# Optimization experiments

Hardware: AMD Instinct MI355X
Metric: run time of the kernel (lower is better)

## Reference

```python
import jax, jax.numpy as jnp
import numpy as np
from jax import lax


def _conv(x, w, b, pad, dil):
    # standard dense conv, NCHW / OIHW
    out = lax.conv_general_dilated(
        x, w, window_strides=(1, 1), padding=[(pad, pad), (pad, pad)],
        rhs_dilation=(dil, dil), dimension_numbers=('NCHW', 'OIHW', 'NCHW'))
    return out + b[None, :, None, None]


def _bilinear_sample(x, py, px):
    # x: [B,C,H,W]; py,px: [B,H,W] float coords. Zero padding outside bounds
    # (matches torchvision deform_conv2d bilinear sampling).
    B, C, H, W = x.shape
    y0 = jnp.floor(py)
    x0 = jnp.floor(px)
    wy = (py - y0)[:, None]  # [B,1,H,W]
    wx = (px - x0)[:, None]
    y0i = y0.astype(jnp.int32)
    x0i = x0.astype(jnp.int32)
    xf = x.reshape(B, C, H * W)

    def gather(yi, xi):
        valid = ((yi >= 0) & (yi < H) & (xi >= 0) & (xi < W))[:, None]
        yc = jnp.clip(yi, 0, H - 1)
        xc = jnp.clip(xi, 0, W - 1)
        idx = jnp.broadcast_to((yc * W + xc).reshape(B, 1, H * W), (B, C, H * W))
        v = jnp.take_along_axis(xf, idx, axis=2).reshape(B, C, H, W)
        return v * valid.astype(x.dtype)

    v00 = gather(y0i, x0i)
    v01 = gather(y0i, x0i + 1)
    v10 = gather(y0i + 1, x0i)
    v11 = gather(y0i + 1, x0i + 1)
    return (v00 * (1 - wy) * (1 - wx) + v01 * (1 - wy) * wx
            + v10 * wy * (1 - wx) + v11 * wy * wx)


def _deform_dw_conv(x, off_w, off_b, dw_w, k, pad, dil):
    # offset net: regular conv -> [B, 2*k*k, H, W] (dy,dx per kernel tap)
    # then depthwise deformable conv with weight dw_w: [C,1,k,k], no bias.
    B, C, H, W = x.shape
    off = _conv(x, off_w, off_b, pad, dil).reshape(B, k * k, 2, H, W)
    ys = jnp.arange(H, dtype=x.dtype)[None, :, None]  # [1,H,1]
    xs = jnp.arange(W, dtype=x.dtype)[None, None, :]  # [1,1,W]
    out = jnp.zeros_like(x)
    for t in range(k * k):  # small fixed tap count (25 or 49)
        ki, kj = t // k, t % k
        py = ys - pad + ki * dil + off[:, t, 0]  # [B,H,W]
        px = xs - pad + kj * dil + off[:, t, 1]
        samp = _bilinear_sample(x, py, px)       # [B,C,H,W]
        out = out + samp * dw_w[:, 0, ki, kj][None, :, None, None]
    return out


def setup_inputs() -> dict:
    key = jax.random.key(0)
    ks = jax.random.split(key, 10)
    B, C, H, W = 8, 64, 128, 128
    x = jax.random.normal(ks[0], (B, C, H, W), dtype=jnp.float32)
    # conv0: DeformConv 5x5, pad=2, dil=1, depthwise
    off0_w = jax.random.normal(ks[1], (2 * 25, C, 5, 5), dtype=jnp.float32) * 0.01
    off0_b = jnp.zeros((2 * 25,), dtype=jnp.float32)
    dw0_w = jax.random.normal(ks[2], (C, 1, 5, 5), dtype=jnp.float32) * (1.0 / 5.0)
    # conv_spatial: DeformConv 7x7, pad=9, dil=3, depthwise
    off1_w = jax.random.normal(ks[3], (2 * 49, C, 7, 7), dtype=jnp.float32) * 0.01
    off1_b = jnp.zeros((2 * 49,), dtype=jnp.float32)
    dw1_w = jax.random.normal(ks[4], (C, 1, 7, 7), dtype=jnp.float32) * (1.0 / 7.0)
    # conv1: 1x1 dense conv with bias
    conv1_w = jax.random.normal(ks[5], (C, C, 1, 1), dtype=jnp.float32) * (1.0 / np.sqrt(C))
    conv1_b = jnp.zeros((C,), dtype=jnp.float32)
    return {"x": x, "off0_w": off0_w, "off0_b": off0_b, "dw0_w": dw0_w,
            "off1_w": off1_w, "off1_b": off1_b, "dw1_w": dw1_w,
            "conv1_w": conv1_w, "conv1_b": conv1_b}


def reference(x, off0_w, off0_b, dw0_w, off1_w, off1_b, dw1_w, conv1_w, conv1_b):
    u = x
    attn = _deform_dw_conv(x, off0_w, off0_b, dw0_w, k=5, pad=2, dil=1)
    attn = _deform_dw_conv(attn, off1_w, off1_b, dw1_w, k=7, pad=9, dil=3)
    attn = jnp.einsum('bchw,oc->bohw', attn, conv1_w[:, :, 0, 0]) + conv1_b[None, :, None, None]
    return u * attn
```

## Files before the change

kernel.cpp:

```cpp
#include <hip/hip_runtime.h>
#include <hip/hip_fp16.h>

#define Bb 8
#define C  64
#define Hh 128
#define Ww 128
#define HW (Hh * Ww)

typedef __attribute__((ext_vector_type(8))) short b16x8;
typedef __attribute__((ext_vector_type(4))) float f32x4;
typedef _Float16 f16x8 __attribute__((ext_vector_type(8)));
typedef __fp16 fp16x2cv __attribute__((ext_vector_type(2)));

__device__ __forceinline__ ushort f2h(float f) {
    union { _Float16 h; ushort u; } z; z.h = (_Float16)f; return z.u;
}
__device__ __forceinline__ uint pkrtz_u(float a, float b) {
    union { fp16x2cv h; uint u; } z;
    z.h = __builtin_amdgcn_cvt_pkrtz(a, b); return z.u;
}
__device__ __forceinline__ f16x8 s2h8(b16x8 s) {
    union { b16x8 s; f16x8 h; } x; x.s = s; return x.h;
}
__device__ __forceinline__ __half2 u2hh(uint u) {
    union { uint u; __half2 h; } x; x.u = u; return x.h;
}
__device__ __forceinline__ uint hh2u(__half2 h) {
    union { uint u; __half2 h; } x; x.h = h; return x.u;
}
__device__ __forceinline__ float h2f_lo(uint u) {
    union { uint u; __half2 h; } x; x.u = u; return __low2float(x.h);
}
__device__ __forceinline__ float h2f_hi(uint u) {
    union { uint u; __half2 h; } x; x.u = u; return __high2float(x.h);
}

__global__ void pack_nhwc(const float* __restrict__ in, ushort* __restrict__ out) {
    __shared__ ushort t[64][65];
    const int bx = blockIdx.x;
    const int b = bx >> 8, rem = bx & 255, h = rem >> 1, w0 = (rem & 1) << 6;
    const int x = threadIdx.x, wl = x & 63, cs = x >> 6;
    const float* ip = in + (((size_t)b * 64) << 14) + (h << 7) + w0 + wl;
    #pragma unroll
    for (int i = 0; i < 16; ++i) {
        const int c = i * 4 + cs;
        t[wl][c] = f2h(ip[(size_t)c << 14]);
    }
    __syncthreads();
    ushort* op = out + ((size_t)((b * Hh + h) * Ww + w0)) * 64 + wl;
    #pragma unroll
    for (int i = 0; i < 16; ++i) {
        const int w = i * 4 + cs;
        op[(size_t)w * 64] = t[w][wl];
    }
}

__global__ void pack_w(const float* __restrict__ src, ushort* __restrict__ dst,
                       int OC, int OCP, int KK, int n) {
    const int idx = blockIdx.x * 256 + threadIdx.x;
    if (idx >= n) return;
    const int kk = idx & 31;
    const int oc = (idx >> 5) % OCP;
    const int s = idx / (32 * OCP);
    const int c = (s & 1) * 32 + kk;
    const int t = s >> 1;
    const float v = (oc < OC) ? src[((size_t)oc * 64 + c) * KK + t] : 0.f;
    dst[idx] = f2h(v);
}

__global__ void pack_dwt(const float* __restrict__ src, ushort* __restrict__ dst, int KK) {
    const int i = blockIdx.x * 256 + threadIdx.x;
    if (i < KK * 64) {
        const int t = i >> 6, ch = i & 63;
        dst[i] = f2h(src[ch * KK + t]);
    }
}

template<int K, int PAD, int DIL, int OCP, int KR>
__global__ __launch_bounds__(256, 4) void conv_mfma(
    const ushort* __restrict__ xp,
    const ushort* __restrict__ wp,
    const float* __restrict__ bias,
    ushort* __restrict__ outp) {
    constexpr int WIDTH = 128 + (K - 1) * DIL;
    constexpr int S = 2 * K * K;
    constexpr int SP = S + 2;
    constexpr int NT = OCP / 16;
    constexpr int TPW = (NT + 3) / 4;
    constexpr int STG = KR * WIDTH * 64;
    constexpr int EPI = 128 * SP;
    constexpr int LN = STG > EPI ? STG : EPI;
    __shared__ __align__(16) ushort lds[LN];

    const int bx = blockIdx.x;
    const int b = bx >> 7, h = bx & 127;
    const int tid = threadIdx.x, lane = tid & 63, wid = tid >> 6;
    const int l15 = lane & 15, lg = lane >> 4;

    f32x4 acc[TPW][8] = {};

    const int nph = (K + KR - 1) / KR;
    for (int ph = 0; ph < nph; ++ph) {
        const int kr0 = ph * KR;
        const int krn = (K - kr0 < KR) ? (K - kr0) : KR;
        __syncthreads();
        const int chunks = krn * WIDTH * 8;
        for (int q = tid; q < chunks; q += 256) {
            const int ki = q / (WIDTH * 8);
            const int r2 = q - ki * (WIDTH * 8);
            const int widx = r2 >> 3, csl = r2 & 7;
            const int y = h - PAD + (kr0 + ki) * DIL;
            const int w = -PAD + widx;
            uint4 v = make_uint4(0, 0, 0, 0);
            if ((unsigned)y < 128u && (unsigned)w < 128u)
                v = *(const uint4*)(xp + (((size_t)(b * 128 + y) * 128 + w) << 6) + (csl << 3));
            ((uint4*)lds)[(ki * WIDTH + widx) * 8 + (csl ^ (widx & 7))] = v;
        }
        __syncthreads();

        const int t1 = (kr0 + krn) * K;
        for (int t = kr0 * K; t < t1; ++t) {
            const int ki = t / K - kr0;
            const int kj = t - (t / K) * K;
            const int s0 = 2 * t;
            b16x8 a[2][TPW];
            #pragma unroll
            for (int i = 0; i < TPW; ++i) {
                if (wid + 4 * i < NT) {
                    const int ot = wid + 4 * i;
                    const size_t ab = ((size_t)(ot * 16 + l15)) * 32 + lg * 8;
                    a[0][i] = *(const b16x8*)(wp + (size_t)s0 * (OCP * 32) + ab);
                    a[1][i] = *(const b16x8*)(wp + (size_t)(s0 + 1) * (OCP * 32) + ab);
                }
            }
            const int wb0 = l15 + kj * DIL;
            int idx = (ki * WIDTH + wb0) * 8 + (lg ^ (wb0 & 7));
            #pragma unroll
            for (int pt = 0; pt < 8; ++pt) {
                const b16x8 b0 = ((const b16x8*)lds)[idx];
                const b16x8 b1 = ((const b16x8*)lds)[idx ^ 4];
                #pragma unroll
                for (int i = 0; i < TPW; ++i) {
                    if (wid + 4 * i < NT) {
                        acc[i][pt] = __builtin_amdgcn_mfma_f32_16x16x32_f16(s2h8(a[0][i]), s2h8(b0), acc[i][pt], 0, 0, 0);
                        acc[i][pt] = __builtin_amdgcn_mfma_f32_16x16x32_f16(s2h8(a[1][i]), s2h8(b1), acc[i][pt], 0, 0, 0);
                    }
                }
                idx += 128;
            }
        }
    }

    __syncthreads();
    #pragma unroll
    for (int i = 0; i < TPW; ++i) {
        const int ot = wid + 4 * i;
        if (ot >= NT) continue;
        #pragma unroll
        for (int r = 0; r < 4; ++r) {
            const int oc = ot * 16 + lg * 4 + r;
            if (oc < S) {
                const float bv = bias[oc];
                #pragma unroll
                for (int pt = 0; pt < 8; ++pt)
                    lds[(pt * 16 + l15) * SP + oc] = f2h(acc[i][pt][r] + bv);
            }
        }
    }
    __syncthreads();
    constexpr int SH = S / 2, SPH = SP / 2;
    const uint* lu = (const uint*)lds;
    uint* og = (uint*)outp + ((size_t)bx << 7) * SH;
    for (int q = tid; q < 128 * SH; q += 256) {
        const int pix = q / SH, s = q - pix * SH;
        og[q] = lu[pix * SPH + s];
    }
}

template <int K, int PAD, int DIL>
__global__ __launch_bounds__(256, 4) void deform5(
    const ushort* __restrict__ xp,
    const ushort* __restrict__ off,
    const ushort* __restrict__ dwt,
    ushort* __restrict__ outb) {
    constexpr int KK = K * K;
    __shared__ ushort dwl[KK * 64];
    __shared__ uint sIdx[32 * KK];
    __shared__ __align__(8) uint2 sW[32 * KK];
    const int tid = threadIdx.x;
    const int pix0 = blockIdx.x * 32;

    for (int i = tid; i < KK * 32; i += 256)
        ((uint*)dwl)[i] = ((const uint*)dwt)[i];

    const uint* og = (const uint*)off + (size_t)pix0 * KK;
    for (int q = tid; q < 32 * KK; q += 256) {
        const int pl2 = q / KK, t2 = q - pl2 * KK;
        const int pix = pix0 + pl2;
        const int h = (pix >> 7) & 127, w = pix & 127;
        const uint od = og[q];
        const int ki = t2 / K, kj = t2 - ki * K;
        const float py = (float)(h - PAD + ki * DIL) + h2f_lo(od);
        const float px = (float)(w - PAD + kj * DIL) + h2f_hi(od);
        const float y0f = floorf(py), x0f = floorf(px);
        const float wy = py - y0f, wx = px - x0f;
        const int y0 = (int)y0f, x0 = (int)x0f;
        const int y1 = y0 + 1, x1 = x0 + 1;
        const float m00 = ((unsigned)y0 < 128u && (unsigned)x0 < 128u) ? 1.f : 0.f;
        const float m01 = ((unsigned)y0 < 128u && (unsigned)x1 < 128u) ? 1.f : 0.f;
        const float m10 = ((unsigned)y1 < 128u && (unsigned)x0 < 128u) ? 1.f : 0.f;
        const float m11 = ((unsigned)y1 < 128u && (unsigned)x1 < 128u) ? 1.f : 0.f;
        const int y0c = min(max(y0, 0), 127), y1c = min(max(y1, 0), 127);
        const int x0c = min(max(x0, 0), 127), x1c = min(max(x1, 0), 127);
        const float w00 = (1.f - wy) * (1.f - wx) * m00;
        const float w01 = (1.f - wy) * wx * m01;
        const float w10 = wy * (1.f - wx) * m10;
        const float w11 = wy * wx * m11;
        const int i00 = (y0c << 7) | x0c;
        const int i11 = (y1c << 7) | x1c;
        const int dx = x1c - x0c;
        sIdx[q] = (uint)i00 | ((uint)i11 << 14) | ((uint)dx << 28);
        sW[q] = make_uint2(pkrtz_u(w00, w01), pkrtz_u(w10, w11));
    }
    __syncthreads();

    const int pl = tid >> 3, g = tid & 7;
    const int pix = pix0 + pl;
    const int bimg = pix0 >> 14;
    const int gb = g << 3;
    const char* xb8 = (const char*)(xp + ((size_t)bimg << 20)) + (gb << 1);
    const int base = pl * KK;

    __half2 acc_h[4] = {};

#define CORNERS(ID, A_, B_, C_, D_)                                          \
    {                                                                        \
        const int i00_ = (ID) & 16383;                                       \
        const int i11_ = ((ID) >> 14) & 16383;                               \
        const int dxb_ = ((ID) >> 21) & 128;                                 \
        const int o00_ = i00_ << 7, o11_ = i11_ << 7;                        \
        A_ = *(const uint4*)(xb8 + o00_);                                    \
        B_ = *(const uint4*)(xb8 + (o00_ + dxb_));                           \
        C_ = *(const uint4*)(xb8 + (o11_ - dxb_));                           \
        D_ = *(const uint4*)(xb8 + o11_);                                    \
    }

#define MATH(T, A_, B_, C_, D_, W_)                                          \
    {                                                                        \
        const __half2 wv0 = u2hh((W_).x), wv1 = u2hh((W_).y);                \
        const __half2 w00b = __low2half2(wv0), w01b = __high2half2(wv0);     \
        const __half2 w10b = __low2half2(wv1), w11b = __high2half2(wv1);     \
        const uint4 dwv = *(const uint4*)(dwl + ((T) << 6) + gb);            \
        const uint* Ap = (const uint*)&(A_);                                 \
        const uint* Bp = (const uint*)&(B_);                                 \
        const uint* Cp = (const uint*)&(C_);                                 \
        const uint* Dp = (const uint*)&(D_);                                 \
        const uint* Wp = (const uint*)&dwv;                                  \
        _Pragma("unroll")                                                    \
        for (int j = 0; j < 4; ++j) {                                        \
            __half2 v = __hmul2(u2hh(Ap[j]), w00b);                          \
            v = __hfma2(u2hh(Bp[j]), w01b, v);                               \
            v = __hfma2(u2hh(Cp[j]), w10b, v);                               \
            v = __hfma2(u2hh(Dp[j]), w11b, v);                               \
            acc_h[j] = __hfma2(v, u2hh(Wp[j]), acc_h[j]);                    \
        }                                                                    \
    }

    uint id0 = sIdx[base];
    uint2 w40 = sW[base];
    uint id1; uint2 w41;
    uint4 A0, B0, C0, D0, A1, B1, C1, D1;
    CORNERS(id0, A0, B0, C0, D0);

    for (int t = 0; t + 1 < KK; t += 2) {
        id1 = sIdx[base + t + 1]; w41 = sW[base + t + 1];
        CORNERS(id1, A1, B1, C1, D1);
        MATH(t, A0, B0, C0, D0, w40);
        if (t + 2 < KK) {
            id0 = sIdx[base + t + 2]; w40 = sW[base + t + 2];
            CORNERS(id0, A0, B0, C0, D0);
        }
        MATH(t + 1, A1, B1, C1, D1, w41);
    }
    MATH(KK - 1, A0, B0, C0, D0, w40);

#undef CORNERS
#undef MATH

    uint o4[4];
    #pragma unroll
    for (int j = 0; j < 4; ++j) o4[j] = hh2u(acc_h[j]);
    *(uint4*)(outb + ((size_t)pix << 6) + gb) = *(uint4*)o4;
}

__global__ __launch_bounds__(256) void pw_mfma(
    const ushort* __restrict__ attn, const ushort* __restrict__ wp2,
    const float* __restrict__ b1, const float* __restrict__ x,
    float* __restrict__ out) {
    __shared__ __align__(16) ushort lds[64 * 64];
    const int tid = threadIdx.x, lane = tid & 63, wid = tid >> 6;
    const int l15 = lane & 15, lg = lane >> 4;
    const int pix0 = blockIdx.x << 6;

    const uint4* src = (const uint4*)(attn + ((size_t)pix0 << 6));
    for (int q = tid; q < 512; q += 256) {
        const int widx = q >> 3, csl = q & 7;
        ((uint4*)lds)[widx * 8 + (csl ^ (widx & 7))] = src[q];
    }
    __syncthreads();

    const b16x8 a0 = *(const b16x8*)(wp2 + ((size_t)(wid * 16 + l15)) * 32 + lg * 8);
    const b16x8 a1 = *(const b16x8*)(wp2 + ((size_t)(64 + wid * 16 + l15)) * 32 + lg * 8);
    f32x4 acc[4] = {};
    #pragma unroll
    for (int pt = 0; pt < 4; ++pt) {
        const int wb = pt * 16 + l15;
        const int idx = wb * 8 + (lg ^ (wb & 7));
        const b16x8 b0 = ((const b16x8*)lds)[idx];
        const b16x8 b1v = ((const b16x8*)lds)[idx ^ 4];
        acc[pt] = __builtin_amdgcn_mfma_f32_16x16x32_f16(s2h8(a0), s2h8(b0), acc[pt], 0, 0, 0);
        acc[pt] = __builtin_amdgcn_mfma_f32_16x16x32_f16(s2h8(a1), s2h8(b1v), acc[pt], 0, 0, 0);
    }

    const int b = pix0 >> 14, hw0 = pix0 & 16383;
    #pragma unroll
    for (int r = 0; r < 4; ++r) {
        const int oc = wid * 16 + lg * 4 + r;
        const float bv = b1[oc];
        const size_t base = (((size_t)b * 64 + oc) << 14) + hw0;
        #pragma unroll
        for (int pt = 0; pt < 4; ++pt) {
            const size_t oi = base + pt * 16 + l15;
            out[oi] = x[oi] * (acc[pt][r] + bv);
        }
    }
}

extern "C" void kernel_launch(void* const* d_in, const int* in_sizes, int n_in,
                              void* d_out, int out_size, void* d_ws, size_t ws_size,
                              hipStream_t stream) {
    const float* x       = (const float*)d_in[0];
    const float* off0_w  = (const float*)d_in[1];
    const float* off0_b  = (const float*)d_in[2];
    const float* dw0_w   = (const float*)d_in[3];
    const float* off1_w  = (const float*)d_in[4];
    const float* off1_b  = (const float*)d_in[5];
    const float* dw1_w   = (const float*)d_in[6];
    const float* conv1_w = (const float*)d_in[7];
    const float* conv1_b = (const float*)d_in[8];
    float* out = (float*)d_out;

    const size_t NPX = (size_t)Bb * HW;
    ushort* xp     = (ushort*)d_ws;
    ushort* attn0b = xp + NPX * 64;
    ushort* attn1b = attn0b + NPX * 64;
    ushort* offb   = attn1b + NPX * 64;
    ushort* wp0    = offb + NPX * 98;
    ushort* wp1    = wp0 + 50 * 64 * 32;
    ushort* wpP    = wp1 + 98 * 112 * 32;
    ushort* dwt0   = wpP + 2 * 64 * 32;
    ushort* dwt1   = dwt0 + 25 * 64;

    const dim3 blk(256);

    pack_nhwc<<<2048, blk, 0, stream>>>(x, xp);
    pack_w<<<(50 * 64 * 32 + 255) / 256, blk, 0, stream>>>(off0_w, wp0, 50, 64, 25, 50 * 64 * 32);
    pack_w<<<(98 * 112 * 32 + 255) / 256, blk, 0, stream>>>(off1_w, wp1, 98, 112, 49, 98 * 112 * 32);
    pack_w<<<16, blk, 0, stream>>>(conv1_w, wpP, 64, 64, 1, 2 * 64 * 32);
    pack_dwt<<<(25 * 64 + 255) / 256, blk, 0, stream>>>(dw0_w, dwt0, 25);
    pack_dwt<<<(49 * 64 + 255) / 256, blk, 0, stream>>>(dw1_w, dwt1, 49);

    conv_mfma<5, 2, 1, 64, 2><<<1024, blk, 0, stream>>>(xp, wp0, off0_b, offb);
    deform5<5, 2, 1><<<4096, blk, 0, stream>>>(xp, offb, dwt0, attn0b);

    conv_mfma<7, 9, 3, 112, 2><<<1024, blk, 0, stream>>>(attn0b, wp1, off1_b, offb);
    deform5<7, 9, 3><<<4096, blk, 0, stream>>>(attn0b, offb, dwt1, attn1b);

    pw_mfma<<<2048, blk, 0, stream>>>(attn1b, wpP, conv1_b, x, out);
}
```

Measured before the change: 308.8 us.

## Split deformable taps across two thread halves with LDS reduction

The deformable depthwise kernel now runs 512 threads per block of 32 pixels. Each half of the block handles half of the kernel taps, and the two partial sums are combined through shared memory. Per-tap sample metadata is packed into one 16-byte record holding precomputed byte offsets and weights, so each tap needs a single LDS load. The manual two-stage software pipeline is replaced with a simple loop. The goal is more memory-level parallelism for the gather loads, at the cost of an extra reduction barrier and losing the explicit prefetch.

```diff
diff --git a/kernel.cpp b/kernel.cpp
--- a/kernel.cpp
+++ b/kernel.cpp
@@ -178,23 +178,26 @@
 }
 
 template <int K, int PAD, int DIL>
-__global__ __launch_bounds__(256, 4) void deform5(
+__global__ __launch_bounds__(512) void deform6(
     const ushort* __restrict__ xp,
     const ushort* __restrict__ off,
     const ushort* __restrict__ dwt,
     ushort* __restrict__ outb) {
     constexpr int KK = K * K;
-    __shared__ ushort dwl[KK * 64];
-    __shared__ uint sIdx[32 * KK];
-    __shared__ __align__(8) uint2 sW[32 * KK];
+    constexpr int H0 = (KK + 1) / 2;
+    constexpr int SSTB = 32 * KK * 16;
+    __shared__ __align__(16) char smem[SSTB + KK * 128];
+    uint4* sST = (uint4*)smem;
+    ushort* dwl = (ushort*)(smem + SSTB);
+
     const int tid = threadIdx.x;
     const int pix0 = blockIdx.x * 32;
 
-    for (int i = tid; i < KK * 32; i += 256)
+    for (int i = tid; i < KK * 32; i += 512)
         ((uint*)dwl)[i] = ((const uint*)dwt)[i];
 
     const uint* og = (const uint*)off + (size_t)pix0 * KK;
-    for (int q = tid; q < 32 * KK; q += 256) {
+    for (int q = tid; q < 32 * KK; q += 512) {
         const int pl2 = q / KK, t2 = q - pl2 * KK;
         const int pix = pix0 + pl2;
         const int h = (pix >> 7) & 127, w = pix & 127;
@@ -216,81 +219,71 @@
         const float w01 = (1.f - wy) * wx * m01;
         const float w10 = wy * (1.f - wx) * m10;
         const float w11 = wy * wx * m11;
-        const int i00 = (y0c << 7) | x0c;
-        const int i11 = (y1c << 7) | x1c;
-        const int dx = x1c - x0c;
-        sIdx[q] = (uint)i00 | ((uint)i11 << 14) | ((uint)dx << 28);
-        sW[q] = make_uint2(pkrtz_u(w00, w01), pkrtz_u(w10, w11));
-    }
-    __syncthreads();
-
-    const int pl = tid >> 3, g = tid & 7;
+        const uint o00b = (uint)(((y0c << 7) | x0c) << 7);
+        const uint o11b = (uint)(((y1c << 7) | x1c) << 7);
+        const uint dxf = (uint)(x1c - x0c) << 24;
+        sST[q] = make_uint4(o00b | dxf, o11b,
+                            pkrtz_u(w00, w01), pkrtz_u(w10, w11));
+    }
+    __syncthreads();
+
+    const int g = tid & 7, pl = (tid >> 3) & 31, half = tid >> 8;
     const int pix = pix0 + pl;
     const int bimg = pix0 >> 14;
-    const int gb = g << 3;
-    const char* xb8 = (const char*)(xp + ((size_t)bimg << 20)) + (gb << 1);
+    const int gb2 = g << 4;
+    const char* xb8 = (const char*)xp + ((size_t)bimg << 21);
     const int base = pl * KK;
+    const int t0 = half ? H0 : 0, t1 = half ? KK : H0;
 
     __half2 acc_h[4] = {};
 
-#define CORNERS(ID, A_, B_, C_, D_)                                          \
-    {                                                                        \
-        const int i00_ = (ID) & 16383;                                       \
-        const int i11_ = ((ID) >> 14) & 16383;                               \
-        const int dxb_ = ((ID) >> 21) & 128;                                 \
-        const int o00_ = i00_ << 7, o11_ = i11_ << 7;                        \
-        A_ = *(const uint4*)(xb8 + o00_);                                    \
-        B_ = *(const uint4*)(xb8 + (o00_ + dxb_));                           \
-        C_ = *(const uint4*)(xb8 + (o11_ - dxb_));                           \
-        D_ = *(const uint4*)(xb8 + o11_);                                    \
-    }
-
-#define MATH(T, A_, B_, C_, D_, W_)                                          \
-    {                                                                        \
-        const __half2 wv0 = u2hh((W_).x), wv1 = u2hh((W_).y);                \
-        const __half2 w00b = __low2half2(wv0), w01b = __high2half2(wv0);     \
-        const __half2 w10b = __low2half2(wv1), w11b = __high2half2(wv1);     \
-        const uint4 dwv = *(const uint4*)(dwl + ((T) << 6) + gb);            \
-        const uint* Ap = (const uint*)&(A_);                                 \
-        const uint* Bp = (const uint*)&(B_);                                 \
-        const uint* Cp = (const uint*)&(C_);                                 \
-        const uint* Dp = (const uint*)&(D_);                                 \
-        const uint* Wp = (const uint*)&dwv;                                  \
-        _Pragma("unroll")                                                    \
-        for (int j = 0; j < 4; ++j) {                                        \
-            __half2 v = __hmul2(u2hh(Ap[j]), w00b);                          \
-            v = __hfma2(u2hh(Bp[j]), w01b, v);                               \
-            v = __hfma2(u2hh(Cp[j]), w10b, v);                               \
-            v = __hfma2(u2hh(Dp[j]), w11b, v);                               \
-            acc_h[j] = __hfma2(v, u2hh(Wp[j]), acc_h[j]);                    \
-        }                                                                    \
-    }
-
-    uint id0 = sIdx[base];
-    uint2 w40 = sW[base];
-    uint id1; uint2 w41;
-    uint4 A0, B0, C0, D0, A1, B1, C1, D1;
-    CORNERS(id0, A0, B0, C0, D0);
-
-    for (int t = 0; t + 1 < KK; t += 2) {
-        id1 = sIdx[base + t + 1]; w41 = sW[base + t + 1];
-        CORNERS(id1, A1, B1, C1, D1);
-        MATH(t, A0, B0, C0, D0, w40);
-        if (t + 2 < KK) {
-            id0 = sIdx[base + t + 2]; w40 = sW[base + t + 2];
-            CORNERS(id0, A0, B0, C0, D0);
-        }
-        MATH(t + 1, A1, B1, C1, D1, w41);
-    }
-    MATH(KK - 1, A0, B0, C0, D0, w40);
-
-#undef CORNERS
-#undef MATH
-
-    uint o4[4];
-    #pragma unroll
-    for (int j = 0; j < 4; ++j) o4[j] = hh2u(acc_h[j]);
-    *(uint4*)(outb + ((size_t)pix << 6) + gb) = *(uint4*)o4;
+    for (int tt = t0; tt < t1; ++tt) {
+        const uint4 st = sST[base + tt];
+        const uint a = st.x;
+        const uint o00 = (a & 0x00FFFFFFu) + gb2;
+        const uint dxb = (a >> 17) & 128u;
+        const uint o11 = st.y + gb2;
+        const __half2 wv0 = u2hh(st.z), wv1 = u2hh(st.w);
+        const __half2 w00b = __low2half2(wv0), w01b = __high2half2(wv0);
+        const __half2 w10b = __low2half2(wv1), w11b = __high2half2(wv1);
+        const uint4 qa = *(const uint4*)(xb8 + o00);
+        const uint4 qb = *(const uint4*)(xb8 + (o00 + dxb));
+        const uint4 qc = *(const uint4*)(xb8 + (o11 - dxb));
+        const uint4 qd = *(const uint4*)(xb8 + o11);
+        const uint4 dwv = *(const uint4*)(dwl + (tt << 6) + (g << 3));
+        const uint* Ap = (const uint*)&qa;
+        const uint* Bp = (const uint*)&qb;
+        const uint* Cp = (const uint*)&qc;
+        const uint* Dp = (const uint*)&qd;
+        const uint* Wp = (const uint*)&dwv;
+        #pragma unroll
+        for (int j = 0; j < 4; ++j) {
+            __half2 v = __hmul2(u2hh(Ap[j]), w00b);
+            v = __hfma2(u2hh(Bp[j]), w01b, v);
+            v = __hfma2(u2hh(Cp[j]), w10b, v);
+            v = __hfma2(u2hh(Dp[j]), w11b, v);
+            acc_h[j] = __hfma2(v, u2hh(Wp[j]), acc_h[j]);
+        }
+    }
+
+    __syncthreads();
+    uint4* red = (uint4*)smem;
+    if (half) {
+        red[tid & 255] = make_uint4(hh2u(acc_h[0]), hh2u(acc_h[1]),
+                                    hh2u(acc_h[2]), hh2u(acc_h[3]));
+    }
+    __syncthreads();
+    if (!half) {
+        const uint4 o = red[tid];
+        acc_h[0] = __hadd2(acc_h[0], u2hh(o.x));
+        acc_h[1] = __hadd2(acc_h[1], u2hh(o.y));
+        acc_h[2] = __hadd2(acc_h[2], u2hh(o.z));
+        acc_h[3] = __hadd2(acc_h[3], u2hh(o.w));
+        uint o4[4];
+        #pragma unroll
+        for (int j = 0; j < 4; ++j) o4[j] = hh2u(acc_h[j]);
+        *(uint4*)(outb + ((size_t)pix << 6) + (g << 3)) = *(uint4*)o4;
+    }
 }
 
 __global__ __launch_bounds__(256) void pw_mfma(
@@ -371,10 +364,10 @@
     pack_dwt<<<(49 * 64 + 255) / 256, blk, 0, stream>>>(dw1_w, dwt1, 49);
 
     conv_mfma<5, 2, 1, 64, 2><<<1024, blk, 0, stream>>>(xp, wp0, off0_b, offb);
-    deform5<5, 2, 1><<<4096, blk, 0, stream>>>(xp, offb, dwt0, attn0b);
+    deform6<5, 2, 1><<<4096, 512, 0, stream>>>(xp, offb, dwt0, attn0b);
 
     conv_mfma<7, 9, 3, 112, 2><<<1024, blk, 0, stream>>>(attn0b, wp1, off1_b, offb);
-    deform5<7, 9, 3><<<4096, blk, 0, stream>>>(attn0b, offb, dwt1, attn1b);
+    deform6<7, 9, 3><<<4096, 512, 0, stream>>>(attn0b, offb, dwt1, attn1b);
 
     pw_mfma<<<2048, blk, 0, stream>>>(attn1b, wpP, conv1_b, x, out);
 }
```

Measured after the change: 311.6 us. About the same (+0.9%).
